# Kernel tuning notes

Hardware: AMD Instinct MI355X
Metric: run time of the kernel (lower is better)

## Reference

```python
import jax, jax.numpy as jnp
import numpy as np

N = 50000      # nodes
E = 400000     # edges (before self-loops)
D_IN = 128
HID = 128
D_OUT = 128
ED = 64        # edge feature dim
SLOPE_GAT = 0.2   # GATConv attention leaky_relu slope
SLOPE_ACT = 0.01  # nn.LeakyReLU default


def _init(key, shape, scale):
    return jax.random.normal(key, shape, dtype=jnp.float32) * scale


def setup_inputs() -> dict:
    key = jax.random.key(0)
    ks = iter(jax.random.split(key, 48))
    inp = {}
    inp["x"] = jax.random.normal(next(ks), (N, D_IN), dtype=jnp.float32)
    inp["edge_index"] = jax.random.randint(next(ks), (2, E), 0, N, dtype=jnp.int32)
    inp["edge_attr"] = jax.random.normal(next(ks), (E, ED), dtype=jnp.float32)
    # 3 GATConv layers (heads=1): lin_src weight, att_src, att_dst, lin_edge weight, att_edge, bias
    for l, din in enumerate([D_IN, HID, HID]):
        s = 1.0 / np.sqrt(din)
        inp[f"W{l}"] = _init(next(ks), (din, HID), s)
        inp[f"as{l}"] = _init(next(ks), (HID,), 0.1)
        inp[f"ad{l}"] = _init(next(ks), (HID,), 0.1)
        inp[f"We{l}"] = _init(next(ks), (ED, HID), 1.0 / np.sqrt(ED))
        inp[f"ae{l}"] = _init(next(ks), (HID,), 0.1)
        inp[f"b{l}"] = jnp.zeros((HID,), jnp.float32)
    inp["vn_w"] = jnp.zeros((HID,), jnp.float32)  # Embedding(1, hidden), init to 0
    sh = 1.0 / np.sqrt(HID)
    # VN MLP 1 (hidden->hidden->hidden) and final VN MLP (hidden->hidden->output)
    inp["m1w1"] = _init(next(ks), (HID, HID), sh); inp["m1b1"] = jnp.zeros((HID,), jnp.float32)
    inp["m1w2"] = _init(next(ks), (HID, HID), sh); inp["m1b2"] = jnp.zeros((HID,), jnp.float32)
    inp["m2w1"] = _init(next(ks), (HID, HID), sh); inp["m2b1"] = jnp.zeros((HID,), jnp.float32)
    inp["m2w2"] = _init(next(ks), (HID, D_OUT), sh); inp["m2b2"] = jnp.zeros((D_OUT,), jnp.float32)
    inp["Wout"] = _init(next(ks), (HID, D_OUT), sh); inp["bout"] = jnp.zeros((D_OUT,), jnp.float32)
    return inp


def _gat(h_in, src, dst, ea, W, a_s, a_d, We, a_e, b):
    """PyG GATConv (heads=1) on edges with self-loops already appended."""
    h = h_in @ W  # [N, HID]
    alpha = jax.nn.leaky_relu((h @ a_s)[src] + (h @ a_d)[dst] + (ea @ We) @ a_e, SLOPE_GAT)
    m = jax.ops.segment_max(alpha, dst, num_segments=N)
    ex = jnp.exp(alpha - m[dst])
    den = jax.ops.segment_sum(ex, dst, num_segments=N)
    coef = ex / den[dst]
    return jax.ops.segment_sum(coef[:, None] * h[src], dst, num_segments=N) + b


def reference(x, edge_index, edge_attr,
              W0, as0, ad0, We0, ae0, b0,
              W1, as1, ad1, We1, ae1, b1,
              W2, as2, ad2, We2, ae2, b2,
              vn_w, m1w1, m1b1, m1w2, m1b2, m2w1, m2b1, m2w2, m2b2,
              Wout, bout):
    src, dst = edge_index[0], edge_index[1]
    # add_self_loops(fill_value='mean'): self-loop edge_attr = mean of incoming edge_attr
    deg = jax.ops.segment_sum(jnp.ones((E,), jnp.float32), dst, num_segments=N)
    loop_attr = jax.ops.segment_sum(edge_attr, dst, num_segments=N) / jnp.maximum(deg, 1.0)[:, None]
    ar = jnp.arange(N, dtype=src.dtype)
    src2 = jnp.concatenate([src, ar])
    dst2 = jnp.concatenate([dst, ar])
    ea = jnp.concatenate([edge_attr, loop_attr], axis=0)

    out = _gat(x, src2, dst2, ea, W0, as0, ad0, We0, ae0, b0)  # no activation after initial
    out = jax.nn.leaky_relu(_gat(out, src2, dst2, ea, W1, as1, ad1, We1, ae1, b1), SLOPE_ACT)
    out = jax.nn.leaky_relu(_gat(out, src2, dst2, ea, W2, as2, ad2, We2, ae2, b2), SLOPE_ACT)

    # batch=None path: global_add_pool(out, None, size=1) + virtualnode_embedding(0)
    vn = jnp.sum(out, axis=0, keepdims=True) + vn_w[None, :]  # [1, HID]
    vn = jax.nn.relu(vn @ m1w1 + m1b1)
    vn = jax.nn.relu(vn @ m1w2 + m1b2)
    vn = jax.nn.relu(vn @ m2w1 + m2b1)
    vn = jax.nn.relu(vn @ m2w2 + m2b2)  # [1, D_OUT]

    node_out = out @ Wout + bout  # [N, D_OUT]
    return (node_out, vn)
```

## Files before the change

### kernel.cpp

```cpp
#include <hip/hip_runtime.h>

#define NN 50000
#define EE 400000
#define HID 128
#define ED 64
#define LDP 136
#define SLOTS 64

typedef __attribute__((ext_vector_type(8))) unsigned short ushort8_t;
typedef __attribute__((ext_vector_type(8))) short short8_t;
typedef __attribute__((ext_vector_type(4))) float f32x4;

static __device__ __forceinline__ unsigned short f2bf(float f) {
  unsigned u = __float_as_uint(f);
  unsigned r = (u + 0x7FFFu + ((u >> 16) & 1u)) >> 16;
  return (unsigned short)r;
}
static __device__ __forceinline__ float bf2f(unsigned short b) {
  return __uint_as_float((unsigned)b << 16);
}


__global__ __launch_bounds__(256) void k_init(
    int* __restrict__ cnt, float* __restrict__ vnsum,
    const float* __restrict__ We0, const float* __restrict__ We1,
    const float* __restrict__ We2, const float* __restrict__ ae0,
    const float* __restrict__ ae1, const float* __restrict__ ae2,
    float* __restrict__ weae) {
  int b = blockIdx.x;
  int t = threadIdx.x;
  if (b < 196) {
    int i = b * 256 + t;
    if (i < NN) cnt[i] = 0;
  } else if (b == 196) {
    if (t < HID) vnsum[t] = 0.f;
  } else {
    if (t >= 192) return;
    int l = t >> 6, j = t & 63;
    const float* We = (l == 0) ? We0 : (l == 1) ? We1 : We2;
    const float* ae = (l == 0) ? ae0 : (l == 1) ? ae1 : ae2;
    float acc = 0.f;
    for (int k = 0; k < HID; ++k) acc += We[j * HID + k] * ae[k];
    weae[l * ED + j] = acc;
  }
}


__global__ __launch_bounds__(256) void k_main(
    const float* __restrict__ edge_attr, const float* __restrict__ weae,
    const int* __restrict__ src, const int* __restrict__ dst,
    int* __restrict__ cnt, float4* __restrict__ escv,
    const float* __restrict__ x, unsigned short* __restrict__ xb,
    const float* __restrict__ W0, const float* __restrict__ W1,
    const float* __restrict__ W2, const float* __restrict__ Wo,
    unsigned short* __restrict__ Wt) {
  int b = blockIdx.x;
  int tid = threadIdx.x;
  if (b < 6250) {
    __shared__ float4 sw[3][16];
    if (tid < 48) ((float4*)sw)[tid] = ((const float4*)weae)[tid];
    __syncthreads();
    int c = tid & 15;
    int r0 = tid >> 4;
    float4 w0 = sw[0][c], w1 = sw[1][c], w2 = sw[2][c];
    float ra0[4], ra1[4], ra2[4];
    int rows[4];
#pragma unroll
    for (int pass = 0; pass < 4; ++pass) {
      int row = b * 64 + pass * 16 + r0;
      rows[pass] = row;
      float a0 = 0.f, a1 = 0.f, a2 = 0.f;
      if (row < EE) {
        float4 v = ((const float4*)edge_attr)[(size_t)row * 16 + c];
        a0 = v.x * w0.x + v.y * w0.y + v.z * w0.z + v.w * w0.w;
        a1 = v.x * w1.x + v.y * w1.y + v.z * w1.z + v.w * w1.w;
        a2 = v.x * w2.x + v.y * w2.y + v.z * w2.z + v.w * w2.w;
      }
#pragma unroll
      for (int o = 1; o < 16; o <<= 1) {
        a0 += __shfl_xor(a0, o, 64);
        a1 += __shfl_xor(a1, o, 64);
        a2 += __shfl_xor(a2, o, 64);
      }
      ra0[pass] = a0;
      ra1[pass] = a1;
      ra2[pass] = a2;
    }
    if (c == 0) {
      int dv[4], sv[4], p[4];
#pragma unroll
      for (int pass = 0; pass < 4; ++pass) {
        if (rows[pass] < EE) {
          dv[pass] = dst[rows[pass]];
          sv[pass] = src[rows[pass]];
        } else {
          dv[pass] = -1;
        }
      }
#pragma unroll
      for (int pass = 0; pass < 4; ++pass) {
        p[pass] = (dv[pass] >= 0) ? atomicAdd(&cnt[dv[pass]], 1) : SLOTS;
      }
#pragma unroll
      for (int pass = 0; pass < 4; ++pass) {
        if (dv[pass] >= 0 && p[pass] < SLOTS - 1) {
          escv[(size_t)dv[pass] * SLOTS + p[pass]] =
              make_float4(ra0[pass], ra1[pass], ra2[pass],
                          __int_as_float(sv[pass]));
        }
      }
    }
  } else if (b < 12500) {
    int i = (b - 6250) * 256 + tid;
    float4 v = ((const float4*)x)[i];
    ushort4 o;
    o.x = f2bf(v.x); o.y = f2bf(v.y); o.z = f2bf(v.z); o.w = f2bf(v.w);
    ((ushort4*)xb)[i] = o;
  } else {
    int idx = (b - 12500) * 256 + tid;
    int m = idx >> 14;
    int rem = idx & 16383;
    int k = rem >> 7;
    int n = rem & 127;
    const float* W = (m == 0) ? W0 : (m == 1) ? W1 : (m == 2) ? W2 : Wo;
    Wt[(size_t)m * 16384 + n * 128 + k] = f2bf(W[k * 128 + n]);
  }
}


__global__ __launch_bounds__(256) void k_gemmA(
    const unsigned short* __restrict__ A, const unsigned short* __restrict__ Bt,
    const float* __restrict__ as_, const float* __restrict__ ad_,
    unsigned short* __restrict__ hb, float* __restrict__ hs,
    float* __restrict__ hd) {
  __shared__ unsigned short sA[64][LDP];
  __shared__ unsigned short sB[128][LDP];
  int tid = threadIdx.x;
  int row0 = blockIdx.x * 64;
  {
    int r = tid >> 2, sg = (tid & 3) * 32;
    int grow = row0 + r;
    const ushort8_t* src = (const ushort8_t*)(A + (size_t)grow * HID + sg);
    ushort8_t z = {0, 0, 0, 0, 0, 0, 0, 0};
#pragma unroll
    for (int i = 0; i < 4; ++i)
      *(ushort8_t*)&sA[r][sg + i * 8] = (grow < NN) ? src[i] : z;
  }
  {
    int r = tid >> 1, sg = (tid & 1) * 64;
    const ushort8_t* src = (const ushort8_t*)(Bt + r * HID + sg);
#pragma unroll
    for (int i = 0; i < 8; ++i) *(ushort8_t*)&sB[r][sg + i * 8] = src[i];
  }
  __syncthreads();
  int w = tid >> 6, l = tid & 63;
  int lr = l & 15, lg = l >> 4;
  f32x4 acc[8] = {};
  const unsigned short* pa = &sA[w * 16 + lr][lg * 8];
  const unsigned short* pb = &sB[lr][lg * 8];
#pragma unroll
  for (int ks = 0; ks < 4; ++ks) {
    short8_t a = *(const short8_t*)(pa + ks * 32);
#pragma unroll
    for (int ct = 0; ct < 8; ++ct) {
      short8_t b = *(const short8_t*)(pb + ct * 16 * LDP + ks * 32);
      acc[ct] = __builtin_amdgcn_mfma_f32_16x16x32_bf16(a, b, acc[ct], 0, 0, 0);
    }
  }
  int orow = row0 + w * 16 + lg * 4;
#pragma unroll
  for (int ct = 0; ct < 8; ++ct) {
    int col = ct * 16 + lr;
#pragma unroll
    for (int r = 0; r < 4; ++r) {
      int grow = orow + r;
      if (grow < NN) hb[(size_t)grow * HID + col] = f2bf(acc[ct][r]);
    }
  }
  float asv[8], adv[8];
#pragma unroll
  for (int ct = 0; ct < 8; ++ct) {
    asv[ct] = as_[ct * 16 + lr];
    adv[ct] = ad_[ct * 16 + lr];
  }
#pragma unroll
  for (int r = 0; r < 4; ++r) {
    float ps = 0.f, pd = 0.f;
#pragma unroll
    for (int ct = 0; ct < 8; ++ct) {
      ps += acc[ct][r] * asv[ct];
      pd += acc[ct][r] * adv[ct];
    }
#pragma unroll
    for (int o = 1; o < 16; o <<= 1) {
      ps += __shfl_xor(ps, o, 64);
      pd += __shfl_xor(pd, o, 64);
    }
    int grow = orow + r;
    if (lr == 0 && grow < NN) {
      hs[grow] = ps;
      hd[grow] = pd;
    }
  }
}

__global__ __launch_bounds__(256) void k_gemmO(
    const unsigned short* __restrict__ A, const unsigned short* __restrict__ Bt,
    const float* __restrict__ bias, float* __restrict__ O,
    float* __restrict__ vnsum) {
  __shared__ unsigned short sA[64][LDP];
  __shared__ unsigned short sB[128][LDP];
  int tid = threadIdx.x;
  int row0 = blockIdx.x * 64;
  {
    int r = tid >> 2, sg = (tid & 3) * 32;
    int grow = row0 + r;
    const ushort8_t* src = (const ushort8_t*)(A + (size_t)grow * HID + sg);
    ushort8_t z = {0, 0, 0, 0, 0, 0, 0, 0};
#pragma unroll
    for (int i = 0; i < 4; ++i)
      *(ushort8_t*)&sA[r][sg + i * 8] = (grow < NN) ? src[i] : z;
  }
  {
    int r = tid >> 1, sg = (tid & 1) * 64;
    const ushort8_t* src = (const ushort8_t*)(Bt + r * HID + sg);
#pragma unroll
    for (int i = 0; i < 8; ++i) *(ushort8_t*)&sB[r][sg + i * 8] = src[i];
  }
  __syncthreads();
  int w = tid >> 6, l = tid & 63;
  int lr = l & 15, lg = l >> 4;
  f32x4 acc[8] = {};
  const unsigned short* pa = &sA[w * 16 + lr][lg * 8];
  const unsigned short* pb = &sB[lr][lg * 8];
#pragma unroll
  for (int ks = 0; ks < 4; ++ks) {
    short8_t a = *(const short8_t*)(pa + ks * 32);
#pragma unroll
    for (int ct = 0; ct < 8; ++ct) {
      short8_t b = *(const short8_t*)(pb + ct * 16 * LDP + ks * 32);
      acc[ct] = __builtin_amdgcn_mfma_f32_16x16x32_bf16(a, b, acc[ct], 0, 0, 0);
    }
  }
  int orow = row0 + w * 16 + lg * 4;
#pragma unroll
  for (int ct = 0; ct < 8; ++ct) {
    int col = ct * 16 + lr;
    float bv = bias[col];
#pragma unroll
    for (int r = 0; r < 4; ++r) {
      int grow = orow + r;
      if (grow < NN) O[(size_t)grow * HID + col] = acc[ct][r] + bv;
    }
  }
  if (tid < HID) {
    float s = 0.f;
#pragma unroll
    for (int r = 0; r < 64; ++r) s += bf2f(sA[r][tid]);
    atomicAdd(&vnsum[tid], s);
  }
}


__global__ __launch_bounds__(256) void k_aggregate7(
    const unsigned short* __restrict__ hb, const float* __restrict__ hs,
    const float* __restrict__ hd, const float4* __restrict__ escv,
    const int* __restrict__ cnt, const float* __restrict__ bias,
    unsigned short* __restrict__ outb, int lsel, int act) {
  int i = blockIdx.x * 4 + (threadIdx.x >> 6);
  int lane = threadIdx.x & 63;
  if (i >= NN) return;
  int g = lane >> 4;
  int j = lane & 15;
  int deg = cnt[i];
  if (deg > SLOTS - 1) deg = SLOTS - 1;
  int nt = deg + 1;
  float hdi = hd[i];
  int t = lane;
  int sv = i;
  float esc_l = 0.f;
  if (t < deg) {
    float4 v = escv[(size_t)i * SLOTS + t];
    sv = __float_as_int(v.w);
    esc_l = (lsel == 0) ? v.x : (lsel == 1) ? v.y : v.z;
  }
  float se = esc_l;
#pragma unroll
  for (int o = 1; o < 64; o <<= 1) se += __shfl_xor(se, o, 64);
  float w = 0.f;
  if (t < nt) {
    float av;
    if (t < deg)
      av = hs[sv] + hdi + esc_l;
    else
      av = hs[i] + hdi + se / (float)(deg > 1 ? deg : 1);
    av = (av > 0.f) ? av : 0.2f * av;
    w = __expf(av);
  }
  float den_l = w;
  float4 acc0 = make_float4(0.f, 0.f, 0.f, 0.f);
  float4 acc1 = make_float4(0.f, 0.f, 0.f, 0.f);
  int q = g;
  if (q < nt) {
    float wq = __shfl(w, q, 64);
    int sq = __shfl(sv, q, 64);
    if (q == deg) sq = i;
    ushort8_t hv = *(const ushort8_t*)(hb + (size_t)sq * HID + j * 8);
    for (int qn = q + 4; qn < nt; qn += 4) {
      float wn = __shfl(w, qn, 64);
      int sn = __shfl(sv, qn, 64);
      if (qn == deg) sn = i;
      ushort8_t hn = *(const ushort8_t*)(hb + (size_t)sn * HID + j * 8);
      acc0.x += wq * bf2f(hv[0]);
      acc0.y += wq * bf2f(hv[1]);
      acc0.z += wq * bf2f(hv[2]);
      acc0.w += wq * bf2f(hv[3]);
      acc1.x += wq * bf2f(hv[4]);
      acc1.y += wq * bf2f(hv[5]);
      acc1.z += wq * bf2f(hv[6]);
      acc1.w += wq * bf2f(hv[7]);
      wq = wn;
      hv = hn;
    }
    acc0.x += wq * bf2f(hv[0]);
    acc0.y += wq * bf2f(hv[1]);
    acc0.z += wq * bf2f(hv[2]);
    acc0.w += wq * bf2f(hv[3]);
    acc1.x += wq * bf2f(hv[4]);
    acc1.y += wq * bf2f(hv[5]);
    acc1.z += wq * bf2f(hv[6]);
    acc1.w += wq * bf2f(hv[7]);
  }
#pragma unroll
  for (int o = 1; o < 64; o <<= 1) den_l += __shfl_xor(den_l, o, 64);
#pragma unroll
  for (int o = 16; o <= 32; o <<= 1) {
    acc0.x += __shfl_xor(acc0.x, o, 64);
    acc0.y += __shfl_xor(acc0.y, o, 64);
    acc0.z += __shfl_xor(acc0.z, o, 64);
    acc0.w += __shfl_xor(acc0.w, o, 64);
    acc1.x += __shfl_xor(acc1.x, o, 64);
    acc1.y += __shfl_xor(acc1.y, o, 64);
    acc1.z += __shfl_xor(acc1.z, o, 64);
    acc1.w += __shfl_xor(acc1.w, o, 64);
  }
  if (g == 0) {
    float inv = 1.f / den_l;
    const float4* bp = (const float4*)(bias + j * 8);
    float4 b0 = bp[0], b1 = bp[1];
    float v[8];
    v[0] = acc0.x * inv + b0.x; v[1] = acc0.y * inv + b0.y;
    v[2] = acc0.z * inv + b0.z; v[3] = acc0.w * inv + b0.w;
    v[4] = acc1.x * inv + b1.x; v[5] = acc1.y * inv + b1.y;
    v[6] = acc1.z * inv + b1.z; v[7] = acc1.w * inv + b1.w;
    ushort8_t ob;
#pragma unroll
    for (int q2 = 0; q2 < 8; ++q2) {
      float tv = v[q2];
      if (act) tv = (tv > 0.f) ? tv : 0.01f * tv;
      ob[q2] = f2bf(tv);
    }
    *(ushort8_t*)(outb + (size_t)i * HID + j * 8) = ob;
  }
}


__global__ void k_mlp(const float* __restrict__ vnsum, const float* __restrict__ vn_w,
                      const float* __restrict__ w1, const float* __restrict__ b1,
                      const float* __restrict__ w2, const float* __restrict__ b2,
                      const float* __restrict__ w3, const float* __restrict__ b3,
                      const float* __restrict__ w4, const float* __restrict__ b4,
                      float* __restrict__ outv) {
  __shared__ float xb[HID], yb[HID];
  int t = threadIdx.x;
  xb[t] = vnsum[t] + vn_w[t];
  __syncthreads();
  const float* Ws[4] = {w1, w2, w3, w4};
  const float* Bs[4] = {b1, b2, b3, b4};
  float* cur = xb;
  float* nxt = yb;
  for (int l = 0; l < 4; ++l) {
    const float* W = Ws[l];
    const float* B = Bs[l];
    float acc = B[t];
    for (int d = 0; d < HID; ++d) acc += cur[d] * W[d * HID + t];
    nxt[t] = fmaxf(acc, 0.f);
    __syncthreads();
    float* tmp = cur; cur = nxt; nxt = tmp;
  }
  outv[t] = cur[t];
}


extern "C" void kernel_launch(void* const* d_in, const int* in_sizes, int n_in,
                              void* d_out, int out_size, void* d_ws, size_t ws_size,
                              hipStream_t stream) {
  const float* x = (const float*)d_in[0];
  const int* ei = (const int*)d_in[1];
  const float* edge_attr = (const float*)d_in[2];
  const float *W[3], *as_[3], *ad_[3], *We[3], *ae[3], *bb[3];
  for (int l = 0; l < 3; ++l) {
    W[l]   = (const float*)d_in[3 + l * 6 + 0];
    as_[l] = (const float*)d_in[3 + l * 6 + 1];
    ad_[l] = (const float*)d_in[3 + l * 6 + 2];
    We[l]  = (const float*)d_in[3 + l * 6 + 3];
    ae[l]  = (const float*)d_in[3 + l * 6 + 4];
    bb[l]  = (const float*)d_in[3 + l * 6 + 5];
  }
  const float* vn_w = (const float*)d_in[21];
  const float* m1w1 = (const float*)d_in[22];
  const float* m1b1 = (const float*)d_in[23];
  const float* m1w2 = (const float*)d_in[24];
  const float* m1b2 = (const float*)d_in[25];
  const float* m2w1 = (const float*)d_in[26];
  const float* m2b1 = (const float*)d_in[27];
  const float* m2w2 = (const float*)d_in[28];
  const float* m2b2 = (const float*)d_in[29];
  const float* Wout = (const float*)d_in[30];
  const float* bout = (const float*)d_in[31];

  char* ws = (char*)d_ws;
  size_t o = 0;
  auto alloc = [&](size_t bytes) {
    o = (o + 255) & ~(size_t)255;
    void* p = ws + o;
    o += bytes;
    return p;
  };
  unsigned short* xb   = (unsigned short*)alloc((size_t)NN * HID * 2);
  unsigned short* hb   = (unsigned short*)alloc((size_t)NN * HID * 2);
  unsigned short* outb = (unsigned short*)alloc((size_t)NN * HID * 2);
  unsigned short* Wtb  = (unsigned short*)alloc((size_t)4 * HID * HID * 2);
  float4* escv   = (float4*)alloc((size_t)NN * SLOTS * 16);
  float* hs     = (float*)alloc((size_t)NN * 4);
  float* hd     = (float*)alloc((size_t)NN * 4);
  float* vnsum  = (float*)alloc(HID * 4);
  float* weae   = (float*)alloc(3 * ED * 4);
  int* cnt      = (int*)alloc((size_t)NN * 4);

  const int* srcv = ei;
  const int* dstv = ei + EE;

  k_init<<<198, 256, 0, stream>>>(cnt, vnsum, We[0], We[1], We[2], ae[0],
                                  ae[1], ae[2], weae);
  k_main<<<12756, 256, 0, stream>>>(edge_attr, weae, srcv, dstv, cnt, escv, x,
                                    xb, W[0], W[1], W[2], Wout, Wtb);

  const unsigned short* in_b = xb;
  for (int l = 0; l < 3; ++l) {
    k_gemmA<<<(NN + 63) / 64, 256, 0, stream>>>(
        in_b, Wtb + (size_t)l * HID * HID, as_[l], ad_[l], hb, hs, hd);
    k_aggregate7<<<(NN + 3) / 4, 256, 0, stream>>>(
        hb, hs, hd, escv, cnt, bb[l], outb, l, (l > 0) ? 1 : 0);
    in_b = outb;
  }

  float* node_out = (float*)d_out;
  k_gemmO<<<(NN + 63) / 64, 256, 0, stream>>>(
      outb, Wtb + (size_t)3 * HID * HID, bout, node_out, vnsum);
  k_mlp<<<1, 128, 0, stream>>>(vnsum, vn_w, m1w1, m1b1, m1w2, m1b2, m2w1, m2b1,
                               m2w2, m2b2, node_out + (size_t)NN * HID);
}
```

Before: 232.5 us.

## Fuse x bf16 conversion and layer-0 GEMM into the edge-preprocessing kernel

Moves the weight transpose/convert into the init kernel, then merges the edge-scatter work with the layer-0 projection GEMM in one launch. The GEMM blocks read fp32 x directly, convert to bf16 in shared memory, and compute h, hs and hd, so the separate xb buffer and the first k_gemmA launch go away. This removes one kernel launch and a full write and read of the bf16 copy of x. In exchange the layer-0 GEMM blocks read B straight from global memory instead of staging it in LDS, and they share a launch with the atomic-heavy edge blocks.

```diff
diff --git a/kernel.cpp b/kernel.cpp
--- a/kernel.cpp
+++ b/kernel.cpp
@@ -26,7 +26,9 @@
     const float* __restrict__ We0, const float* __restrict__ We1,
     const float* __restrict__ We2, const float* __restrict__ ae0,
     const float* __restrict__ ae1, const float* __restrict__ ae2,
-    float* __restrict__ weae) {
+    float* __restrict__ weae, const float* __restrict__ W0,
+    const float* __restrict__ W1, const float* __restrict__ W2,
+    const float* __restrict__ Wo, unsigned short* __restrict__ Wt) {
   int b = blockIdx.x;
   int t = threadIdx.x;
   if (b < 196) {
@@ -34,7 +36,7 @@
     if (i < NN) cnt[i] = 0;
   } else if (b == 196) {
     if (t < HID) vnsum[t] = 0.f;
-  } else {
+  } else if (b == 197) {
     if (t >= 192) return;
     int l = t >> 6, j = t & 63;
     const float* We = (l == 0) ? We0 : (l == 1) ? We1 : We2;
@@ -42,27 +44,36 @@
     float acc = 0.f;
     for (int k = 0; k < HID; ++k) acc += We[j * HID + k] * ae[k];
     weae[l * ED + j] = acc;
-  }
-}
-
-
-__global__ __launch_bounds__(256) void k_main(
+  } else {
+    int idx = (b - 198) * 256 + t;
+    int m = idx >> 14;
+    int rem = idx & 16383;
+    int k = rem >> 7;
+    int n = rem & 127;
+    const float* W = (m == 0) ? W0 : (m == 1) ? W1 : (m == 2) ? W2 : Wo;
+    Wt[(size_t)m * 16384 + n * 128 + k] = f2bf(W[k * 128 + n]);
+  }
+}
+
+
+__global__ __launch_bounds__(256) void k_l0(
     const float* __restrict__ edge_attr, const float* __restrict__ weae,
     const int* __restrict__ src, const int* __restrict__ dst,
     int* __restrict__ cnt, float4* __restrict__ escv,
-    const float* __restrict__ x, unsigned short* __restrict__ xb,
-    const float* __restrict__ W0, const float* __restrict__ W1,
-    const float* __restrict__ W2, const float* __restrict__ Wo,
-    unsigned short* __restrict__ Wt) {
+    const float* __restrict__ x, const unsigned short* __restrict__ Bt,
+    const float* __restrict__ as_, const float* __restrict__ ad_,
+    unsigned short* __restrict__ hb, float* __restrict__ hs,
+    float* __restrict__ hd) {
+  __shared__ unsigned short shmem[64 * LDP];
   int b = blockIdx.x;
   int tid = threadIdx.x;
   if (b < 6250) {
-    __shared__ float4 sw[3][16];
-    if (tid < 48) ((float4*)sw)[tid] = ((const float4*)weae)[tid];
+    float4* sw = (float4*)shmem;
+    if (tid < 48) sw[tid] = ((const float4*)weae)[tid];
     __syncthreads();
     int c = tid & 15;
     int r0 = tid >> 4;
-    float4 w0 = sw[0][c], w1 = sw[1][c], w2 = sw[2][c];
+    float4 w0 = sw[c], w1 = sw[16 + c], w2 = sw[32 + c];
     float ra0[4], ra1[4], ra2[4];
     int rows[4];
 #pragma unroll
@@ -110,20 +121,76 @@
         }
       }
     }
-  } else if (b < 12500) {
-    int i = (b - 6250) * 256 + tid;
-    float4 v = ((const float4*)x)[i];
-    ushort4 o;
-    o.x = f2bf(v.x); o.y = f2bf(v.y); o.z = f2bf(v.z); o.w = f2bf(v.w);
-    ((ushort4*)xb)[i] = o;
   } else {
-    int idx = (b - 12500) * 256 + tid;
-    int m = idx >> 14;
-    int rem = idx & 16383;
-    int k = rem >> 7;
-    int n = rem & 127;
-    const float* W = (m == 0) ? W0 : (m == 1) ? W1 : (m == 2) ? W2 : Wo;
-    Wt[(size_t)m * 16384 + n * 128 + k] = f2bf(W[k * 128 + n]);
+    unsigned short* sA = shmem;
+    int row0 = (b - 6250) * 64;
+    {
+      int r = tid >> 2, sg = (tid & 3) * 32;
+      int grow = row0 + r;
+      const float4* srcf = (const float4*)(x + (size_t)grow * HID + sg);
+#pragma unroll
+      for (int i = 0; i < 8; ++i) {
+        ushort4 o4 = {0, 0, 0, 0};
+        if (grow < NN) {
+          float4 v = srcf[i];
+          o4.x = f2bf(v.x);
+          o4.y = f2bf(v.y);
+          o4.z = f2bf(v.z);
+          o4.w = f2bf(v.w);
+        }
+        *(ushort4*)&sA[r * LDP + sg + i * 4] = o4;
+      }
+    }
+    __syncthreads();
+    int w = tid >> 6, l = tid & 63;
+    int lr = l & 15, lg = l >> 4;
+    f32x4 acc[8] = {};
+    const unsigned short* pa = &sA[(w * 16 + lr) * LDP + lg * 8];
+#pragma unroll
+    for (int ks = 0; ks < 4; ++ks) {
+      short8_t a = *(const short8_t*)(pa + ks * 32);
+#pragma unroll
+      for (int ct = 0; ct < 8; ++ct) {
+        short8_t bf =
+            *(const short8_t*)(Bt + (ct * 16 + lr) * HID + ks * 32 + lg * 8);
+        acc[ct] = __builtin_amdgcn_mfma_f32_16x16x32_bf16(a, bf, acc[ct], 0, 0, 0);
+      }
+    }
+    int orow = row0 + w * 16 + lg * 4;
+#pragma unroll
+    for (int ct = 0; ct < 8; ++ct) {
+      int col = ct * 16 + lr;
+#pragma unroll
+      for (int r = 0; r < 4; ++r) {
+        int grow = orow + r;
+        if (grow < NN) hb[(size_t)grow * HID + col] = f2bf(acc[ct][r]);
+      }
+    }
+    float asv[8], adv[8];
+#pragma unroll
+    for (int ct = 0; ct < 8; ++ct) {
+      asv[ct] = as_[ct * 16 + lr];
+      adv[ct] = ad_[ct * 16 + lr];
+    }
+#pragma unroll
+    for (int r = 0; r < 4; ++r) {
+      float ps = 0.f, pd = 0.f;
+#pragma unroll
+      for (int ct = 0; ct < 8; ++ct) {
+        ps += acc[ct][r] * asv[ct];
+        pd += acc[ct][r] * adv[ct];
+      }
+#pragma unroll
+      for (int o = 1; o < 16; o <<= 1) {
+        ps += __shfl_xor(ps, o, 64);
+        pd += __shfl_xor(pd, o, 64);
+      }
+      int grow = orow + r;
+      if (lr == 0 && grow < NN) {
+        hs[grow] = ps;
+        hd[grow] = pd;
+      }
+    }
   }
 }
 
@@ -427,7 +494,6 @@
     o += bytes;
     return p;
   };
-  unsigned short* xb   = (unsigned short*)alloc((size_t)NN * HID * 2);
   unsigned short* hb   = (unsigned short*)alloc((size_t)NN * HID * 2);
   unsigned short* outb = (unsigned short*)alloc((size_t)NN * HID * 2);
   unsigned short* Wtb  = (unsigned short*)alloc((size_t)4 * HID * HID * 2);
@@ -441,18 +507,19 @@
   const int* srcv = ei;
   const int* dstv = ei + EE;
 
-  k_init<<<198, 256, 0, stream>>>(cnt, vnsum, We[0], We[1], We[2], ae[0],
-                                  ae[1], ae[2], weae);
-  k_main<<<12756, 256, 0, stream>>>(edge_attr, weae, srcv, dstv, cnt, escv, x,
-                                    xb, W[0], W[1], W[2], Wout, Wtb);
-
-  const unsigned short* in_b = xb;
-  for (int l = 0; l < 3; ++l) {
+  k_init<<<454, 256, 0, stream>>>(cnt, vnsum, We[0], We[1], We[2], ae[0],
+                                  ae[1], ae[2], weae, W[0], W[1], W[2], Wout,
+                                  Wtb);
+  k_l0<<<7032, 256, 0, stream>>>(edge_attr, weae, srcv, dstv, cnt, escv, x,
+                                 Wtb, as_[0], ad_[0], hb, hs, hd);
+
+  k_aggregate7<<<(NN + 3) / 4, 256, 0, stream>>>(hb, hs, hd, escv, cnt, bb[0],
+                                                 outb, 0, 0);
+  for (int l = 1; l < 3; ++l) {
     k_gemmA<<<(NN + 63) / 64, 256, 0, stream>>>(
-        in_b, Wtb + (size_t)l * HID * HID, as_[l], ad_[l], hb, hs, hd);
+        outb, Wtb + (size_t)l * HID * HID, as_[l], ad_[l], hb, hs, hd);
     k_aggregate7<<<(NN + 3) / 4, 256, 0, stream>>>(
-        hb, hs, hd, escv, cnt, bb[l], outb, l, (l > 0) ? 1 : 0);
-    in_b = outb;
+        hb, hs, hd, escv, cnt, bb[l], outb, l, 1);
   }
 
   float* node_out = (float*)d_out;
```

Measured after the change: 236.9 us. No clear change (+1.9%).
